# Kernel tuning notes

Measured on AMD Instinct MI355X. Metric: run time of the kernel, lower is better.

## Reference

```python
import jax, jax.numpy as jnp
import numpy as np

EMBED_DIM = 2048
NUM_HEADS = 16
HEAD_DIM = EMBED_DIM // NUM_HEADS  # 128
D_K = 128
SCALE = 1.0 / float(np.sqrt(HEAD_DIM))
LAYER_DEPTH = 6 / 12  # amrpa_layer_idx / n_amrpa_layers
BATCH, SEQ = 2, 2048


def setup_inputs() -> dict:
    key = jax.random.key(0)
    ks = jax.random.split(key, 8)
    return {
        "hidden_states": jax.random.normal(ks[0], (BATCH, SEQ, EMBED_DIM), jnp.float32),
        "c_attn_w": jax.random.normal(ks[1], (EMBED_DIM, 3 * EMBED_DIM), jnp.float32) * 0.02,
        "c_attn_b": jax.random.normal(ks[2], (3 * EMBED_DIM,), jnp.float32) * 0.02,
        "c_proj_w": jax.random.normal(ks[3], (EMBED_DIM, EMBED_DIM), jnp.float32) * 0.02,
        "c_proj_b": jax.random.normal(ks[4], (EMBED_DIM,), jnp.float32) * 0.02,
        "cam_gate": jax.random.normal(ks[5], (D_K,), jnp.float32) * 0.1,
        "cam_w0": jax.random.normal(ks[6], (1,), jnp.float32),
        "cam_w1": jax.random.normal(ks[7], (1,), jnp.float32),
    }


def reference(hidden_states, c_attn_w, c_attn_b, c_proj_w, c_proj_b, cam_gate, cam_w0, cam_w1):
    # GPT2 Conv1D-style fused QKV projection: [B,S,3E]
    qkv = hidden_states @ c_attn_w + c_attn_b
    Q, K, V = jnp.split(qkv, 3, axis=2)  # each [B,S,E]
    # NOTE: faithful to source — attention over the FULL embed dim (no head split),
    # scaled by 1/sqrt(head_dim); causal mask is computed but never applied upstream.
    attn_scores = jnp.einsum('bse,bte->bst', Q, K) * SCALE  # [B,S,S]

    # CAM: sliced low-rank channels
    Q_cam, K_cam, V_cam = Q[:, :, :D_K], K[:, :, :D_K], V[:, :, :D_K]
    # base attention map computed under no_grad in the original
    base_A = jax.lax.stop_gradient(
        jax.nn.softmax(jnp.einsum('bsd,btd->bst', Q_cam, K_cam) * SCALE, axis=-1))
    layer_weight = jax.nn.sigmoid(cam_w0[0] + cam_w1[0] * LAYER_DEPTH)
    cam_ctx = jnp.einsum('bst,btd->bsd', base_A, V_cam)            # [B,S,d_k]
    cam_bias = jnp.einsum('bsd,btd->bst', jnp.tanh(cam_ctx * cam_gate), K_cam)
    cam_bias = cam_bias * (SCALE * layer_weight)                   # cam_mask is all-ones

    final_attn = jax.nn.softmax(attn_scores + cam_bias, axis=-1)
    context = jnp.einsum('bst,bte->bse', final_attn, V)            # [B,S,E]
    output = context @ c_proj_w + c_proj_b                         # resid_dropout is identity (eval)
    return output
```

## Files before the change

kernel.cpp:

```cpp
#include <hip/hip_runtime.h>
#include <hip/hip_bf16.h>

typedef unsigned short u16;
typedef __attribute__((ext_vector_type(8))) __bf16 bf16x8;
typedef __attribute__((ext_vector_type(4))) float f32x4;
typedef __attribute__((ext_vector_type(4))) unsigned short u16x4;

#define SCALE_QK 0.08838834764831845f

__device__ __forceinline__ u16 f2bf(float x) {
  union { float f; unsigned u; } v; v.f = x;
  unsigned r = v.u + 0x7fffu + ((v.u >> 16) & 1u);
  return (u16)(r >> 16);
}

__device__ __forceinline__ void gload_lds16(const u16* g, u16* l) {
  __builtin_amdgcn_global_load_lds(
      (const __attribute__((address_space(1))) unsigned*)g,
      (__attribute__((address_space(3))) unsigned*)l, 16, 0, 0);
}

#define CFENCE() asm volatile("" ::: "memory")
#define WAITV(N) asm volatile("s_waitcnt vmcnt(" #N ")" ::: "memory")

template<bool OUT_BF16, bool HAS_BIAS>
__global__ __launch_bounds__(512, 2)
void g128p(const u16* __restrict__ A1, int lda, long sA1,
           const u16* __restrict__ B1, int ldb, long sB1, int K,
           void* __restrict__ Cv, int ldc, long sC,
           float scale, const float* __restrict__ bias, int nbx,
           int mapmode, u16* __restrict__ vTout)
{
  extern __shared__ u16 lds[];
  const int bz = blockIdx.z;
  const int nwg = gridDim.x, orig = blockIdx.x;
  const int q8 = nwg >> 3, r8 = nwg & 7;
  const int xcd = orig & 7, lp = orig >> 3;
  const int wg = (xcd < r8 ? xcd * (q8 + 1) : r8 * (q8 + 1) + (xcd - r8) * q8) + lp;
  int bx, by;
  if (mapmode == 1) {
    const int x = wg / 96, c = wg % 96;
    const int rect = c / 48, i6 = c % 48;
    by = rect * 8 + (i6 & 7);
    bx = x * 6 + (i6 >> 3);
  } else {
    by = wg / nbx; bx = wg % nbx;
  }
  const long m0 = (long)by * 256, n0 = (long)bx * 128;

  const int tid = threadIdx.x, wid = tid >> 6, lane = tid & 63;
  const int wm = wid >> 1, wn = wid & 1;
  const int rl = lane & 15, g = lane >> 4;
  const int sw = ((g ^ ((rl >> 1) & 3)) << 3);

  int aoff[4], boff[4];
#pragma unroll
  for (int i = 0; i < 4; ++i) aoff[i] = (wm * 64 + i * 16 + rl) * 32 + sw;
#pragma unroll
  for (int j = 0; j < 4; ++j) boff[j] = (wn * 64 + j * 16 + rl) * 32 + sw;

  const int srow = tid >> 2;
  const int scolX = (((tid & 3) ^ ((srow >> 1) & 3)) << 3);

  f32x4 acc[4][4];
#pragma unroll
  for (int i = 0; i < 4; ++i)
#pragma unroll
    for (int j = 0; j < 4; ++j) acc[i][j] = (f32x4){0.f, 0.f, 0.f, 0.f};

  bf16x8 avA[4], bvA[4], avB[4], bvB[4];

  const u16* Ab = A1 + (long)bz * sA1 + m0 * (long)lda;
  const u16* Bb = B1 + (long)bz * sB1 + n0 * (long)ldb;

#define STG(H_) {                                                        \
    const int h_ = (H_);                                                 \
    const u16* sa_ = Ab + (long)srow * lda + h_ * 32 + scolX;            \
    u16* da_ = lds + ((h_ & 3) * 8192) + tid * 8;                        \
    gload_lds16(sa_, da_);                                               \
    gload_lds16(sa_ + (long)128 * lda, da_ + 4096);                      \
    gload_lds16(Bb + (long)srow * ldb + h_ * 32 + scolX,                 \
                lds + 32768 + ((h_ & 3) * 4096) + tid * 8); }
#define RD(H_, AV, BV) {                                                 \
    const u16* aS_ = lds + (((H_) & 3) * 8192);                          \
    const u16* bS_ = lds + 32768 + (((H_) & 3) * 4096);                  \
    _Pragma("unroll") for (int i_ = 0; i_ < 4; ++i_)                     \
      AV[i_] = *(const bf16x8*)(aS_ + aoff[i_]);                         \
    _Pragma("unroll") for (int j_ = 0; j_ < 4; ++j_)                     \
      BV[j_] = *(const bf16x8*)(bS_ + boff[j_]); }
#define BODY(K_, CAV, CBV, NAV, NBV, W_STMT, DO_RD, DO_ST)               \
    W_STMT;                                                              \
    CFENCE(); __builtin_amdgcn_s_barrier(); CFENCE();                    \
    asm volatile("s_waitcnt lgkmcnt(0)" ::: "memory");                   \
    __builtin_amdgcn_sched_barrier(0);                                   \
    __builtin_amdgcn_s_setprio(1);                                       \
    _Pragma("unroll") for (int i_ = 0; i_ < 4; ++i_)                     \
      _Pragma("unroll") for (int j_ = 0; j_ < 4; ++j_)                   \
        acc[i_][j_] = __builtin_amdgcn_mfma_f32_16x16x32_bf16(           \
            CAV[i_], CBV[j_], acc[i_][j_], 0, 0, 0);                     \
    __builtin_amdgcn_s_setprio(0);                                       \
    if (DO_RD) { RD((K_) + 1, NAV, NBV); }                               \
    if (DO_ST) { STG((K_) + 4); }                                        \
    CFENCE();

  const int H = K >> 5;

  STG(0); STG(1); STG(2);
  WAITV(6);
  CFENCE(); __builtin_amdgcn_s_barrier(); CFENCE();
  RD(0, avA, bvA);
  STG(3);
  CFENCE();

#pragma unroll 1
  for (int k = 0; k + 5 < H; k += 2) {
    BODY(k,     avA, bvA, avB, bvB, WAITV(6), true, true);
    BODY(k + 1, avB, bvB, avA, bvA, WAITV(6), true, true);
  }
  BODY(H - 4, avA, bvA, avB, bvB, WAITV(6), true,  false);
  BODY(H - 3, avB, bvB, avA, bvA, WAITV(3), true,  false);
  BODY(H - 2, avA, bvA, avB, bvB, WAITV(0), true,  false);
  BODY(H - 1, avB, bvB, avA, bvA, (void)0,  false, false);
#undef STG
#undef RD
#undef BODY

  const int r0 = (lane >> 4) << 2;
  const int cL = lane & 15;
#pragma unroll
  for (int i = 0; i < 4; ++i) {
#pragma unroll
    for (int j = 0; j < 4; ++j) {
      const long row = m0 + wm * 64 + i * 16 + r0;
      const long col = n0 + wn * 64 + j * 16 + cL;
      float bvs = 0.f;
      if (HAS_BIAS) bvs = bias[col];
      if (OUT_BF16) {
        u16* Cp = (u16*)Cv + (long)bz * sC;
        if (vTout && col >= 4096) {
          u16x4 tq;
#pragma unroll
          for (int r = 0; r < 4; ++r) tq[r] = f2bf(acc[i][j][r] * scale + bvs);
          *(u16x4*)(vTout + ((long)(row >> 11) * 2048 + (col - 4096)) * 2048 + (row & 2047)) = tq;
        } else {
#pragma unroll
          for (int r = 0; r < 4; ++r)
            Cp[(row + r) * ldc + col] = f2bf(acc[i][j][r] * scale + bvs);
        }
      } else {
        float* Cp = (float*)Cv + (long)bz * sC;
#pragma unroll
        for (int r = 0; r < 4; ++r)
          Cp[(row + r) * ldc + col] = acc[i][j][r] * scale + bvs;
      }
    }
  }
}

template<bool OUT_BF16, bool HAS_BIAS, bool TWO_SEG>
__global__ __launch_bounds__(512, 2)
void g128q(const u16* __restrict__ A1, int lda1, long sA1,
           const u16* __restrict__ B1, int ldb1, long sB1, int K1,
           const u16* __restrict__ A2, int lda2, long sA2,
           const u16* __restrict__ B2, int ldb2, long sB2, int K2,
           void* __restrict__ Cv, int ldc, long sC,
           float scale, const float* __restrict__ bias, int nbx)
{
  extern __shared__ u16 lds[];
  const int bz = blockIdx.z;
  const int nwg = gridDim.x, orig = blockIdx.x;
  const int q8 = nwg >> 3, r8 = nwg & 7;
  const int xcd = orig & 7, lp = orig >> 3;
  const int wg = (xcd < r8 ? xcd * (q8 + 1) : r8 * (q8 + 1) + (xcd - r8) * q8) + lp;
  const int bx = wg % nbx, by = wg / nbx;
  const long m0 = (long)by * 256, n0 = (long)bx * 128;

  const int tid = threadIdx.x, wid = tid >> 6, lane = tid & 63;
  const int wm = wid >> 1, wn = wid & 1;
  const int rl = lane & 15, g = lane >> 4;
  const int xa = rl & 7;
  const int uk0 = ((g ^ xa) << 3);
  const int uk1 = (((4 + g) ^ xa) << 3);

  int aoffb[4], boffb[4];
#pragma unroll
  for (int i = 0; i < 4; ++i) aoffb[i] = (wm * 64 + i * 16 + rl) * 64;
#pragma unroll
  for (int j = 0; j < 4; ++j) boffb[j] = 16384 + (wn * 64 + j * 16 + rl) * 64;

  const int ra = tid >> 3;
  const int xcol = (((tid & 7) ^ ((tid >> 3) & 7)) << 3);

  f32x4 acc[4][4];
#pragma unroll
  for (int i = 0; i < 4; ++i)
#pragma unroll
    for (int j = 0; j < 4; ++j) acc[i][j] = (f32x4){0.f, 0.f, 0.f, 0.f};

  bf16x8 av[2][4], bv[2][2];

#define STG(T_, BO_) { const int k0_ = (T_) << 6;                        \
    gload_lds16(Ab + (long)(ra      ) * lda + k0_ + xcol, lds + (BO_) +         tid * 8); \
    gload_lds16(Ab + (long)(ra +  64) * lda + k0_ + xcol, lds + (BO_) +  4096 + tid * 8); \
    gload_lds16(Ab + (long)(ra + 128) * lda + k0_ + xcol, lds + (BO_) +  8192 + tid * 8); \
    gload_lds16(Ab + (long)(ra + 192) * lda + k0_ + xcol, lds + (BO_) + 12288 + tid * 8); \
    gload_lds16(Bb + (long)(ra      ) * ldb + k0_ + xcol, lds + (BO_) + 16384 + tid * 8); \
    gload_lds16(Bb + (long)(ra +  64) * ldb + k0_ + xcol, lds + (BO_) + 20480 + tid * 8); }
#define RD0(BO_) { const u16* p_ = lds + (BO_);                          \
    _Pragma("unroll") for (int i_ = 0; i_ < 4; ++i_) {                   \
      av[0][i_] = *(const bf16x8*)(p_ + aoffb[i_] + uk0);                \
      av[1][i_] = *(const bf16x8*)(p_ + aoffb[i_] + uk1); }              \
    _Pragma("unroll") for (int j_ = 0; j_ < 2; ++j_) {                   \
      bv[0][j_] = *(const bf16x8*)(p_ + boffb[j_] + uk0);                \
      bv[1][j_] = *(const bf16x8*)(p_ + boffb[j_] + uk1); } }
#define RD1(BO_) { const u16* p_ = lds + (BO_);                          \
    _Pragma("unroll") for (int j_ = 0; j_ < 2; ++j_) {                   \
      bv[0][j_] = *(const bf16x8*)(p_ + boffb[2 + j_] + uk0);            \
      bv[1][j_] = *(const bf16x8*)(p_ + boffb[2 + j_] + uk1); } }
#define MMPH(JB_)                                                        \
    CFENCE(); __builtin_amdgcn_s_barrier();                              \
    asm volatile("s_waitcnt lgkmcnt(0)" ::: "memory");                   \
    __builtin_amdgcn_sched_barrier(0);                                   \
    __builtin_amdgcn_s_setprio(1);                                       \
    _Pragma("unroll") for (int k_ = 0; k_ < 2; ++k_)                     \
      _Pragma("unroll") for (int i_ = 0; i_ < 4; ++i_)                   \
        _Pragma("unroll") for (int j_ = 0; j_ < 2; ++j_)                 \
          acc[i_][(JB_) + j_] = __builtin_amdgcn_mfma_f32_16x16x32_bf16( \
              av[k_][i_], bv[k_][j_], acc[i_][(JB_) + j_], 0, 0, 0);     \
    __builtin_amdgcn_s_setprio(0);                                       \
    CFENCE(); __builtin_amdgcn_s_barrier(); CFENCE();

  const int NSEG = TWO_SEG ? 2 : 1;
#pragma unroll 1
  for (int seg = 0; seg < NSEG; ++seg) {
    const int lda = (seg == 0) ? lda1 : lda2;
    const int ldb = (seg == 0) ? ldb1 : ldb2;
    const int K   = (seg == 0) ? K1 : K2;
    const u16* Ab = ((seg == 0) ? A1 + (long)bz * sA1 : A2 + (long)bz * sA2) + m0 * (long)lda;
    const u16* Bb = ((seg == 0) ? B1 + (long)bz * sB1 : B2 + (long)bz * sB2) + n0 * (long)ldb;
    const int NT = K >> 6;

    STG(0, 0); STG(1, 24576);
    WAITV(6);
    CFENCE(); __builtin_amdgcn_s_barrier(); CFENCE();

    int bo = 0;
#pragma unroll 1
    for (int t = 0; t < NT; ++t) {
      RD0(bo);
      if (t + 2 < NT) {
        int bos = bo - 24576; if (bos < 0) bos = 49152;
        STG(t + 2, bos);
        WAITV(6);
      } else if (t + 1 < NT) {
        WAITV(0);
      }
      MMPH(0)
      RD1(bo);
      MMPH(2)
      bo += 24576; if (bo == 73728) bo = 0;
    }
  }
#undef STG
#undef RD0
#undef RD1
#undef MMPH

  const int r0 = (lane >> 4) << 2;
  const int cL = lane & 15;
#pragma unroll
  for (int i = 0; i < 4; ++i) {
#pragma unroll
    for (int j = 0; j < 4; ++j) {
      const long row = m0 + wm * 64 + i * 16 + r0;
      const long col = n0 + wn * 64 + j * 16 + cL;
      float bvs = 0.f;
      if (HAS_BIAS) bvs = bias[col];
      if (OUT_BF16) {
        u16* Cp = (u16*)Cv + (long)bz * sC;
#pragma unroll
        for (int r = 0; r < 4; ++r)
          Cp[(row + r) * ldc + col] = f2bf(acc[i][j][r] * scale + bvs);
      } else {
        float* Cp = (float*)Cv + (long)bz * sC;
#pragma unroll
        for (int r = 0; r < 4; ++r)
          Cp[(row + r) * ldc + col] = acc[i][j][r] * scale + bvs;
      }
    }
  }
}

__global__ __launch_bounds__(256)
void gemm_bt_splitk(const u16* __restrict__ A, int lda, long sA,
                    const u16* __restrict__ B, int ldb, long sB,
                    float* __restrict__ C, int ldc, long sC,
                    int Kslice, float scale)
{
  __shared__ u16 As[128 * 64];
  __shared__ u16 Bs[128 * 64];
  const int ks = blockIdx.z & 7;
  const int bz = blockIdx.z >> 3;
  const u16* Ap  = A + (long)bz * sA + ks * Kslice;
  const u16* Bp  = B + (long)bz * sB + ks * Kslice;
  const int tid  = threadIdx.x;
  const int wid  = tid >> 6;
  const int lane = tid & 63;
  const long m0  = (long)blockIdx.y * 128;
  const long n0  = (long)blockIdx.x * 128;
  const int lrow = lane >> 3;
  const int lk   = (lane & 7) << 3;
  const int wr   = wid >> 1, wc = wid & 1;

  f32x4 acc[4][4];
#pragma unroll
  for (int i = 0; i < 4; ++i)
#pragma unroll
    for (int j = 0; j < 4; ++j) acc[i][j] = (f32x4){0.f, 0.f, 0.f, 0.f};

  for (int k0 = 0; k0 < Kslice; k0 += 64) {
#pragma unroll
    for (int c4 = 0; c4 < 4; ++c4) {
      const int chunk = (wid << 2) + c4;
      gload_lds16(Ap + (m0 + (chunk << 3) + lrow) * lda + k0 + lk, &As[chunk << 9]);
      gload_lds16(Bp + (n0 + (chunk << 3) + lrow) * ldb + k0 + lk, &Bs[chunk << 9]);
    }
    __syncthreads();
#pragma unroll
    for (int kk = 0; kk < 2; ++kk) {
      bf16x8 af[4], bfr[4];
      const int kof   = (kk << 5) + ((lane >> 4) << 3);
      const int rbase = lane & 15;
#pragma unroll
      for (int i = 0; i < 4; ++i)
        af[i] = *(const bf16x8*)&As[(((wr << 6) + (i << 4) + rbase) << 6) + kof];
#pragma unroll
      for (int j = 0; j < 4; ++j)
        bfr[j] = *(const bf16x8*)&Bs[(((wc << 6) + (j << 4) + rbase) << 6) + kof];
#pragma unroll
      for (int i = 0; i < 4; ++i)
#pragma unroll
        for (int j = 0; j < 4; ++j)
          acc[i][j] = __builtin_amdgcn_mfma_f32_16x16x32_bf16(af[i], bfr[j], acc[i][j], 0, 0, 0);
    }
    __syncthreads();
  }

  const int r0 = (lane >> 4) << 2;
  const int cL = lane & 15;
  float* Cp = C + (long)bz * sC;
#pragma unroll
  for (int i = 0; i < 4; ++i) {
#pragma unroll
    for (int j = 0; j < 4; ++j) {
      const long row = m0 + (wr << 6) + (i << 4) + r0;
      const long col = n0 + (wc << 6) + (j << 4) + cL;
#pragma unroll
      for (int r = 0; r < 4; ++r)
        atomicAdd(&Cp[(row + r) * ldc + col], acc[i][j][r] * scale);
    }
  }
}

__global__ __launch_bounds__(256)
void softmax_rows2048(const float* __restrict__ src, u16* __restrict__ dst) {
  const long row = blockIdx.x;
  const float4* s = (const float4*)(src + row * 2048);
  const int tid = threadIdx.x;
  float4 a = s[tid * 2], b = s[tid * 2 + 1];
  float m = fmaxf(fmaxf(fmaxf(a.x, a.y), fmaxf(a.z, a.w)),
                  fmaxf(fmaxf(b.x, b.y), fmaxf(b.z, b.w)));
#pragma unroll
  for (int o = 32; o > 0; o >>= 1) m = fmaxf(m, __shfl_xor(m, o));
  __shared__ float redm[4];
  __shared__ float reds[4];
  if ((tid & 63) == 0) redm[tid >> 6] = m;
  __syncthreads();
  m = fmaxf(fmaxf(redm[0], redm[1]), fmaxf(redm[2], redm[3]));
  float e[8];
  e[0] = __expf(a.x - m); e[1] = __expf(a.y - m); e[2] = __expf(a.z - m); e[3] = __expf(a.w - m);
  e[4] = __expf(b.x - m); e[5] = __expf(b.y - m); e[6] = __expf(b.z - m); e[7] = __expf(b.w - m);
  float sum = e[0] + e[1] + e[2] + e[3] + e[4] + e[5] + e[6] + e[7];
#pragma unroll
  for (int o = 32; o > 0; o >>= 1) sum += __shfl_xor(sum, o);
  if ((tid & 63) == 0) reds[tid >> 6] = sum;
  __syncthreads();
  sum = reds[0] + reds[1] + reds[2] + reds[3];
  const float inv = 1.f / sum;
  u16x4 o1 = { f2bf(e[0] * inv), f2bf(e[1] * inv), f2bf(e[2] * inv), f2bf(e[3] * inv) };
  u16x4 o2 = { f2bf(e[4] * inv), f2bf(e[5] * inv), f2bf(e[6] * inv), f2bf(e[7] * inv) };
  u16x4* d = (u16x4*)(dst + row * 2048);
  d[tid * 2]     = o1;
  d[tid * 2 + 1] = o2;
}

__global__ void transpose_f32_to_bf16(const float* __restrict__ src, u16* __restrict__ dst,
                                      int R, int C) {
  __shared__ float t[32][33];
  const int c0 = blockIdx.x * 32, r0 = blockIdx.y * 32;
  const int tx = threadIdx.x, ty = threadIdx.y;
#pragma unroll
  for (int i = 0; i < 4; ++i)
    t[ty + i * 8][tx] = src[(long)(r0 + ty + i * 8) * C + c0 + tx];
  __syncthreads();
#pragma unroll
  for (int i = 0; i < 4; ++i)
    dst[(long)(c0 + ty + i * 8) * R + r0 + tx] = f2bf(t[tx][ty + i * 8]);
}

__global__ __launch_bounds__(256)
void convert_f32_to_bf16(const float* __restrict__ src, u16* __restrict__ dst, long n4) {
  long i = (long)blockIdx.x * 256 + threadIdx.x;
  if (i < n4) {
    float4 v = ((const float4*)src)[i];
    *(u16x4*)(dst + i * 4) = (u16x4){ f2bf(v.x), f2bf(v.y), f2bf(v.z), f2bf(v.w) };
  }
}

__global__ __launch_bounds__(256)
void cam_tanh_kernel(const float* __restrict__ ctx, const float* __restrict__ gate,
                     const float* __restrict__ w0, const float* __restrict__ w1,
                     u16* __restrict__ out, int n) {
  int i = blockIdx.x * 256 + threadIdx.x;
  if (i < n) {
    const float lw = 1.f / (1.f + __expf(-(w0[0] + 0.5f * w1[0])));
    int d = i & 127;
    out[i] = f2bf(tanhf(ctx[i] * gate[d]) * lw);
  }
}

__global__ __launch_bounds__(256)
void zero_f32(float* __restrict__ p, int n) {
  int i = blockIdx.x * 256 + threadIdx.x;
  if (i < n) p[i] = 0.f;
}

extern "C" void kernel_launch(void* const* d_in, const int* in_sizes, int n_in,
                              void* d_out, int out_size, void* d_ws, size_t ws_size,
                              hipStream_t stream) {
  const float* hs       = (const float*)d_in[0];
  const float* c_attn_w = (const float*)d_in[1];
  const float* c_attn_b = (const float*)d_in[2];
  const float* c_proj_w = (const float*)d_in[3];
  const float* c_proj_b = (const float*)d_in[4];
  const float* cam_gate = (const float*)d_in[5];
  const float* cam_w0   = (const float*)d_in[6];
  const float* cam_w1   = (const float*)d_in[7];
  float* out = (float*)d_out;

  char* w = (char*)d_ws;
  u16*   hs_b    = (u16*)(w + 256);
  u16*   waT_b   = (u16*)(w + 256 + 16777216UL);
  u16*   wpT_b   = (u16*)(w + 256 + 41943040UL);
  u16*   qkv_b   = (u16*)(w + 256 + 50331648UL);
  u16*   vT_b    = (u16*)(w + 256 + 100663296UL);
  float* scoresF = (float*)(w + 256 + 117440512UL);
  float* camS    = (float*)(w + 256 + 150994944UL);
  float* ctxF    = (float*)(w + 256 + 184549376UL);
  u16*   camT_b  = (u16*)(w + 256 + 186646528UL);
  u16* baseA_b = hs_b;
  u16* P_b     = (u16*)camS;
  u16* ctxE_b  = (u16*)scoresF;

  dim3 b256(256);
  const int LDSP = 98304;
  const int LDSQ = 147456;

  hipFuncSetAttribute((const void*)g128p<true, true>,
                      hipFuncAttributeMaxDynamicSharedMemorySize, LDSP);
  hipFuncSetAttribute((const void*)g128q<false, false, false>,
                      hipFuncAttributeMaxDynamicSharedMemorySize, LDSQ);
  hipFuncSetAttribute((const void*)g128q<false, false, true>,
                      hipFuncAttributeMaxDynamicSharedMemorySize, LDSQ);
  hipFuncSetAttribute((const void*)g128q<true, false, false>,
                      hipFuncAttributeMaxDynamicSharedMemorySize, LDSQ);
  hipFuncSetAttribute((const void*)g128q<false, true, false>,
                      hipFuncAttributeMaxDynamicSharedMemorySize, LDSQ);

  convert_f32_to_bf16<<<dim3(8192), b256, 0, stream>>>(hs, hs_b, 2097152L);
  transpose_f32_to_bf16<<<dim3(192, 64), dim3(32, 8), 0, stream>>>(c_attn_w, waT_b, 2048, 6144);
  transpose_f32_to_bf16<<<dim3(64, 64), dim3(32, 8), 0, stream>>>(c_proj_w, wpT_b, 2048, 2048);

  g128p<true, true><<<dim3(768, 1, 1), dim3(512), LDSP, stream>>>(
      hs_b, 2048, 0L, waT_b, 2048, 0L, 2048,
      qkv_b, 6144, 0L, 1.f, c_attn_b, 48, 1, vT_b);

  g128q<false, false, false><<<dim3(128, 1, 2), dim3(512), LDSQ, stream>>>(
      qkv_b, 6144, 2048L * 6144, qkv_b + 2048, 6144, 2048L * 6144, 128,
      nullptr, 0, 0L, nullptr, 0, 0L, 0,
      camS, 2048, 2048L * 2048, SCALE_QK, nullptr, 16);

  softmax_rows2048<<<dim3(4096), b256, 0, stream>>>(camS, baseA_b);

  zero_f32<<<dim3(2048), b256, 0, stream>>>(ctxF, 524288);
  gemm_bt_splitk<<<dim3(1, 16, 16), b256, 0, stream>>>(
      baseA_b, 2048, 2048L * 2048, vT_b, 2048, 2048L * 2048,
      ctxF, 128, 2048L * 128, 256, 1.f);

  cam_tanh_kernel<<<dim3(2048), b256, 0, stream>>>(ctxF, cam_gate, cam_w0, cam_w1,
                                                   camT_b, 524288);

  g128q<false, false, true><<<dim3(128, 1, 2), dim3(512), LDSQ, stream>>>(
      qkv_b, 6144, 2048L * 6144, qkv_b + 2048, 6144, 2048L * 6144, 2048,
      camT_b, 128, 2048L * 128, qkv_b + 2048, 6144, 2048L * 6144, 128,
      scoresF, 2048, 2048L * 2048, SCALE_QK, nullptr, 16);

  softmax_rows2048<<<dim3(4096), b256, 0, stream>>>(scoresF, P_b);

  g128q<true, false, false><<<dim3(128, 1, 2), dim3(512), LDSQ, stream>>>(
      P_b, 2048, 2048L * 2048, vT_b, 2048, 2048L * 2048, 2048,
      nullptr, 0, 0L, nullptr, 0, 0L, 0,
      ctxE_b, 2048, 2048L * 2048, 1.f, nullptr, 16);

  g128q<false, true, false><<<dim3(256, 1, 1), dim3(512), LDSQ, stream>>>(
      ctxE_b, 2048, 0L, wpT_b, 2048, 0L, 2048,
      nullptr, 0, 0L, nullptr, 0, 0L, 0,
      out, 2048, 0L, 1.f, c_proj_b, 16);
}
```

Baseline: 341.4 us.

## Fuse CAM score GEMM and row softmax into one register-resident kernel

Replaces the separate CAM QK^T GEMM (fp32 scores written to global) and the row softmax kernel with a single kernel. Each block computes 16 full rows of scores in MFMA accumulators, reduces max and sum across waves through shared memory, and writes normalized bf16 probabilities directly. This removes the fp32 score round trip to memory and one launch. The cost is 128 accumulator registers per thread and K loaded straight from global with no LDS staging, and only 256 blocks in the grid.

```diff
diff --git a/kernel.cpp b/kernel.cpp
--- a/kernel.cpp
+++ b/kernel.cpp
@@ -292,6 +292,99 @@
 }
 
 __global__ __launch_bounds__(256)
+void cam_score_softmax(const u16* __restrict__ qkv, u16* __restrict__ baseA)
+{
+  const int bz = blockIdx.z;
+  const long r0 = (long)blockIdx.x * 16;
+  const int tid = threadIdx.x, wv = tid >> 6, lane = tid & 63;
+  const int cs = wv * 512;
+  const int rl = lane & 15, g = lane >> 4;
+
+  const u16* Qb = qkv + (long)bz * 2048 * 6144;
+  const u16* Kb = Qb + 2048;
+
+  bf16x8 av[4];
+#pragma unroll
+  for (int kk = 0; kk < 4; ++kk)
+    av[kk] = *(const bf16x8*)(Qb + (r0 + rl) * 6144 + kk * 32 + g * 8);
+
+  f32x4 acc[32];
+#pragma unroll
+  for (int jt = 0; jt < 32; ++jt) acc[jt] = (f32x4){0.f, 0.f, 0.f, 0.f};
+
+#pragma unroll 4
+  for (int jt = 0; jt < 32; ++jt) {
+    const long t = cs + jt * 16 + rl;
+#pragma unroll
+    for (int kk = 0; kk < 4; ++kk) {
+      bf16x8 bfr = *(const bf16x8*)(Kb + t * 6144 + kk * 32 + g * 8);
+      acc[jt] = __builtin_amdgcn_mfma_f32_16x16x32_bf16(av[kk], bfr, acc[jt], 0, 0, 0);
+    }
+  }
+
+#pragma unroll
+  for (int jt = 0; jt < 32; ++jt)
+#pragma unroll
+    for (int r = 0; r < 4; ++r) acc[jt][r] *= SCALE_QK;
+
+  __shared__ float redm[4][16];
+  __shared__ float reds[4][16];
+
+  float M[4], S[4];
+#pragma unroll
+  for (int r = 0; r < 4; ++r) {
+    float m = acc[0][r];
+#pragma unroll
+    for (int jt = 1; jt < 32; ++jt) m = fmaxf(m, acc[jt][r]);
+#pragma unroll
+    for (int o = 1; o < 16; o <<= 1) m = fmaxf(m, __shfl_xor(m, o));
+    M[r] = m;
+  }
+  if (rl == 0) {
+#pragma unroll
+    for (int r = 0; r < 4; ++r) redm[wv][g * 4 + r] = M[r];
+  }
+  __syncthreads();
+#pragma unroll
+  for (int r = 0; r < 4; ++r)
+    M[r] = fmaxf(fmaxf(redm[0][g * 4 + r], redm[1][g * 4 + r]),
+                 fmaxf(redm[2][g * 4 + r], redm[3][g * 4 + r]));
+#pragma unroll
+  for (int r = 0; r < 4; ++r) S[r] = 0.f;
+#pragma unroll
+  for (int jt = 0; jt < 32; ++jt)
+#pragma unroll
+    for (int r = 0; r < 4; ++r) {
+      float e = __expf(acc[jt][r] - M[r]);
+      acc[jt][r] = e;
+      S[r] += e;
+    }
+#pragma unroll
+  for (int r = 0; r < 4; ++r) {
+#pragma unroll
+    for (int o = 1; o < 16; o <<= 1) S[r] += __shfl_xor(S[r], o);
+  }
+  if (rl == 0) {
+#pragma unroll
+    for (int r = 0; r < 4; ++r) reds[wv][g * 4 + r] = S[r];
+  }
+  __syncthreads();
+#pragma unroll
+  for (int r = 0; r < 4; ++r)
+    S[r] = 1.f / (reds[0][g * 4 + r] + reds[1][g * 4 + r] +
+                  reds[2][g * 4 + r] + reds[3][g * 4 + r]);
+
+  u16* dst = baseA + ((long)bz * 2048 + r0) * 2048;
+#pragma unroll 4
+  for (int jt = 0; jt < 32; ++jt) {
+    const int col = cs + jt * 16 + rl;
+#pragma unroll
+    for (int r = 0; r < 4; ++r)
+      dst[(long)(g * 4 + r) * 2048 + col] = f2bf(acc[jt][r] * S[r]);
+  }
+}
+
+__global__ __launch_bounds__(256)
 void gemm_bt_splitk(const u16* __restrict__ A, int lda, long sA,
                     const u16* __restrict__ B, int ldb, long sB,
                     float* __restrict__ C, int ldc, long sC,
@@ -468,8 +561,6 @@
 
   hipFuncSetAttribute((const void*)g128p<true, true>,
                       hipFuncAttributeMaxDynamicSharedMemorySize, LDSP);
-  hipFuncSetAttribute((const void*)g128q<false, false, false>,
-                      hipFuncAttributeMaxDynamicSharedMemorySize, LDSQ);
   hipFuncSetAttribute((const void*)g128q<false, false, true>,
                       hipFuncAttributeMaxDynamicSharedMemorySize, LDSQ);
   hipFuncSetAttribute((const void*)g128q<true, false, false>,
@@ -485,12 +576,7 @@
       hs_b, 2048, 0L, waT_b, 2048, 0L, 2048,
       qkv_b, 6144, 0L, 1.f, c_attn_b, 48, 1, vT_b);
 
-  g128q<false, false, false><<<dim3(128, 1, 2), dim3(512), LDSQ, stream>>>(
-      qkv_b, 6144, 2048L * 6144, qkv_b + 2048, 6144, 2048L * 6144, 128,
-      nullptr, 0, 0L, nullptr, 0, 0L, 0,
-      camS, 2048, 2048L * 2048, SCALE_QK, nullptr, 16);
-
-  softmax_rows2048<<<dim3(4096), b256, 0, stream>>>(camS, baseA_b);
+  cam_score_softmax<<<dim3(128, 1, 2), b256, 0, stream>>>(qkv_b, baseA_b);
 
   zero_f32<<<dim3(2048), b256, 0, stream>>>(ctxF, 524288);
   gemm_bt_splitk<<<dim3(1, 16, 16), b256, 0, stream>>>(
```

Result: slower. 371.4 us (+8.8%).
